# Kernel optimization log

Hardware: AMD Instinct MI355X
Metric: run time of the kernel (lower is better)

Reference implementation:

```python
import jax, jax.numpy as jnp
import numpy as np

BN_EPS = 1e-5      # torch BatchNorm2d default eps
NORM_EPS = 1e-12   # torch F.normalize default eps


def conv1x1_bn(x, W, b, gamma, beta, mean, var):
    # 1x1 conv == channel matmul; BN in eval mode (running stats)
    y = jnp.einsum('oc,nchw->nohw', W, x) + b[None, :, None, None]
    scale = gamma / jnp.sqrt(var + BN_EPS)
    shift = beta - mean * scale
    return y * scale[None, :, None, None] + shift[None, :, None, None]


def _l2norm(x, axis):
    n = jnp.sqrt(jnp.sum(x * x, axis=axis, keepdims=True))
    return x / jnp.maximum(n, NORM_EPS)


def setup_inputs() -> dict:
    key = jax.random.key(0)
    ks = jax.random.split(key, 16)
    N, C, H, W = 16, 64, 256, 256
    QK = 32
    d = {}
    d['x'] = jax.random.normal(ks[0], (N, C, H, W), jnp.float32)
    # Q projection (C -> 32) + BN
    d['Wq'] = jax.random.normal(ks[1], (QK, C), jnp.float32) * (1.0 / np.sqrt(C))
    d['bq'] = jax.random.normal(ks[2], (QK,), jnp.float32) * 0.01
    d['q_gamma'] = jnp.ones((QK,), jnp.float32)
    d['q_beta'] = jnp.zeros((QK,), jnp.float32)
    d['q_mean'] = jax.random.normal(ks[3], (QK,), jnp.float32) * 0.1
    d['q_var'] = jax.random.uniform(ks[4], (QK,), jnp.float32, 0.5, 1.5)
    # K projection (C -> 32) + BN
    d['Wk'] = jax.random.normal(ks[5], (QK, C), jnp.float32) * (1.0 / np.sqrt(C))
    d['bk'] = jax.random.normal(ks[6], (QK,), jnp.float32) * 0.01
    d['k_gamma'] = jnp.ones((QK,), jnp.float32)
    d['k_beta'] = jnp.zeros((QK,), jnp.float32)
    d['k_mean'] = jax.random.normal(ks[7], (QK,), jnp.float32) * 0.1
    d['k_var'] = jax.random.uniform(ks[8], (QK,), jnp.float32, 0.5, 1.5)
    # V projection (C -> C) + BN
    d['Wv'] = jax.random.normal(ks[9], (C, C), jnp.float32) * (1.0 / np.sqrt(C))
    d['bv'] = jax.random.normal(ks[10], (C,), jnp.float32) * 0.01
    d['v_gamma'] = jnp.ones((C,), jnp.float32)
    d['v_beta'] = jnp.zeros((C,), jnp.float32)
    d['v_mean'] = jax.random.normal(ks[11], (C,), jnp.float32) * 0.1
    d['v_var'] = jax.random.uniform(ks[12], (C,), jnp.float32, 0.5, 1.5)
    # output conv-BN-ReLU (C -> C)
    d['Wo'] = jax.random.normal(ks[13], (C, C), jnp.float32) * (1.0 / np.sqrt(C))
    d['bo'] = jax.random.normal(ks[14], (C,), jnp.float32) * 0.01
    d['o_gamma'] = jnp.ones((C,), jnp.float32)
    d['o_beta'] = jnp.zeros((C,), jnp.float32)
    d['o_mean'] = jax.random.normal(ks[15], (C,), jnp.float32) * 0.1
    d['o_var'] = jax.random.uniform(jax.random.fold_in(key, 99), (C,), jnp.float32, 0.5, 1.5)
    return d


def reference(x, Wq, bq, q_gamma, q_beta, q_mean, q_var,
              Wk, bk, k_gamma, k_beta, k_mean, k_var,
              Wv, bv, v_gamma, v_beta, v_mean, v_var,
              Wo, bo, o_gamma, o_beta, o_mean, o_var):
    N, C, H, W = x.shape
    HW = H * W
    Qm = conv1x1_bn(x, Wq, bq, q_gamma, q_beta, q_mean, q_var)   # [N,32,H,W]
    Km = conv1x1_bn(x, Wk, bk, k_gamma, k_beta, k_mean, k_var)   # [N,32,H,W]
    V0 = conv1x1_bn(x, Wv, bv, v_gamma, v_beta, v_mean, v_var)   # [N,C,H,W]

    Q = jnp.transpose(Qm.reshape(N, 32, HW), (0, 2, 1))          # [N,HW,32]
    Q = _l2norm(Q, axis=2)
    K = _l2norm(Km.reshape(N, 32, HW), axis=1)                   # [N,32,HW]
    V = jax.nn.relu(jnp.transpose(V0.reshape(N, C, HW), (0, 2, 1)))  # [N,HW,C]

    f = jnp.einsum('nks,nsc->nkc', K, V)                         # [N,32,C]
    y = jnp.einsum('nsk,nkc->nsc', Q, f)                         # [N,HW,C]
    y = jnp.transpose(y, (0, 2, 1)).reshape(N, C, H, W)

    out = jax.nn.relu(conv1x1_bn(y, Wo, bo, o_gamma, o_beta, o_mean, o_var))
    return out + V0
```

## Files before the change

kernel.cpp:

```cpp
#include <hip/hip_runtime.h>

#define HW 65536
#define NBATCH 16
#define CCH 64
#define QKC 32

#define OFF_WQT 0
#define OFF_BQ  2048
#define OFF_WKT 2080
#define OFF_BK  4128
#define OFF_WVT 4160
#define OFF_BV  8256
#define OFF_WO  8320
#define OFF_BO  12416
#define OFF_F   12544
#define OFF_MT  45312

#define BPN_A 128
#define BPN_B 128
#define NIT_A ((HW / 64) / BPN_A)
#define NIT_B ((HW / 64) / BPN_B)

typedef __attribute__((ext_vector_type(4))) float f32x4;
typedef __attribute__((ext_vector_type(8))) short bf16x8;
typedef __attribute__((ext_vector_type(4))) short bf16x4;

#define MFMA_P(a, b, c) __builtin_amdgcn_mfma_f32_16x16x32_bf16(a, b, c, 0, 0, 0)
#define MFMA_O(a, b, c) __builtin_amdgcn_mfma_f32_16x16x16bf16_1k(a, b, c, 0, 0, 0)

__device__ __forceinline__ short f2bf(float f) {
    __bf16 h = (__bf16)f;
    return __builtin_bit_cast(short, h);
}

__global__ __launch_bounds__(256) void k0_fold(
    const float* __restrict__ Wq, const float* __restrict__ bq,
    const float* __restrict__ qg, const float* __restrict__ qb,
    const float* __restrict__ qm, const float* __restrict__ qv,
    const float* __restrict__ Wk, const float* __restrict__ bk,
    const float* __restrict__ kg, const float* __restrict__ kb,
    const float* __restrict__ km, const float* __restrict__ kvar,
    const float* __restrict__ Wv, const float* __restrict__ bv,
    const float* __restrict__ vg, const float* __restrict__ vb,
    const float* __restrict__ vm, const float* __restrict__ vvar,
    const float* __restrict__ Wo, const float* __restrict__ bo,
    const float* __restrict__ og, const float* __restrict__ ob,
    const float* __restrict__ om, const float* __restrict__ ovar,
    float* __restrict__ ws)
{
    const int idx = blockIdx.x * 256 + threadIdx.x;
    if (idx < 2048) {
        const int c = idx >> 5, i = idx & 31;
        const float s = qg[i] * rsqrtf(qv[i] + 1e-5f);
        ws[OFF_WQT + idx] = Wq[i * 64 + c] * s;
    } else if (idx < 2080) {
        const int i = idx - 2048;
        const float s = qg[i] * rsqrtf(qv[i] + 1e-5f);
        ws[OFF_BQ + i] = bq[i] * s + qb[i] - qm[i] * s;
    } else if (idx < 4128) {
        const int t = idx - 2080;
        const int c = t >> 5, i = t & 31;
        const float s = kg[i] * rsqrtf(kvar[i] + 1e-5f);
        ws[OFF_WKT + t] = Wk[i * 64 + c] * s;
    } else if (idx < 4160) {
        const int i = idx - 4128;
        const float s = kg[i] * rsqrtf(kvar[i] + 1e-5f);
        ws[OFF_BK + i] = bk[i] * s + kb[i] - km[i] * s;
    } else if (idx < 8256) {
        const int t = idx - 4160;
        const int c = t >> 6, o = t & 63;
        const float s = vg[o] * rsqrtf(vvar[o] + 1e-5f);
        ws[OFF_WVT + t] = Wv[o * 64 + c] * s;
    } else if (idx < 8320) {
        const int o = idx - 8256;
        const float s = vg[o] * rsqrtf(vvar[o] + 1e-5f);
        ws[OFF_BV + o] = bv[o] * s + vb[o] - vm[o] * s;
    } else if (idx < 12416) {
        const int t = idx - 8320;
        const int c = t >> 6, j = t & 63;
        const float s = og[c] * rsqrtf(ovar[c] + 1e-5f);
        ws[OFF_WO + t] = Wo[c * 64 + j] * s;
    } else if (idx < 12480) {
        const int c = idx - 12416;
        const float s = og[c] * rsqrtf(ovar[c] + 1e-5f);
        ws[OFF_BO + c] = bo[c] * s + ob[c] - om[c] * s;
    } else if (idx < 12480 + 32768) {
        ws[OFF_F + (idx - 12480)] = 0.0f;
    }
}

__global__ __launch_bounds__(256) void k1_passA(const float* __restrict__ x,
                                                const float* __restrict__ wsc,
                                                float* __restrict__ f)
{
    __shared__ float red[4 * 2048];

    const int tid = threadIdx.x;
    const int w = tid >> 6;
    const int lane = tid & 63;
    const int ln = lane & 15;
    const int lg = lane >> 4;

    const int n = blockIdx.x / BPN_A;
    const int bslot = blockIdx.x % BPN_A;
    const float* xn = x + (size_t)n * CCH * HW;

    bf16x8 wkf[2][2];
#pragma unroll
    for (int kk = 0; kk < 2; kk++)
#pragma unroll
        for (int t = 0; t < 2; t++) {
            bf16x8 a;
#pragma unroll
            for (int j = 0; j < 8; j++)
                a[j] = f2bf(wsc[OFF_WKT + (kk * 32 + lg * 8 + j) * 32 + t * 16 + ln]);
            wkf[kk][t] = a;
        }
    bf16x8 wvf[2][4];
#pragma unroll
    for (int kk = 0; kk < 2; kk++)
#pragma unroll
        for (int t = 0; t < 4; t++) {
            bf16x8 a;
#pragma unroll
            for (int j = 0; j < 8; j++)
                a[j] = f2bf(wsc[OFF_WVT + (kk * 32 + lg * 8 + j) * 64 + t * 16 + ln]);
            wvf[kk][t] = a;
        }
    float bkb[2], bvb[4];
#pragma unroll
    for (int t = 0; t < 2; t++) bkb[t] = wsc[OFF_BK + t * 16 + ln];
#pragma unroll
    for (int t = 0; t < 4; t++) bvb[t] = wsc[OFF_BV + t * 16 + ln];

    f32x4 facc[2][4];
#pragma unroll
    for (int t = 0; t < 2; t++)
#pragma unroll
        for (int vt = 0; vt < 4; vt++) facc[t][vt] = (f32x4){0.f, 0.f, 0.f, 0.f};

    const int span0 = bslot * NIT_A;

    float xf[16];
    {
        const int sbase = span0 * 64 + w * 16;
#pragma unroll
        for (int kk = 0; kk < 2; kk++) {
            const float* xp = xn + (size_t)(kk * 32 + lg * 8) * HW + sbase + ln;
#pragma unroll
            for (int j = 0; j < 8; j++) xf[kk * 8 + j] = xp[j * HW];
        }
    }

#pragma unroll
    for (int it = 0; it < NIT_A; ++it) {
        float xf2[16];
        if (it + 1 < NIT_A) {
            const int sb2 = (span0 + it + 1) * 64 + w * 16;
#pragma unroll
            for (int kk = 0; kk < 2; kk++) {
                const float* xp = xn + (size_t)(kk * 32 + lg * 8) * HW + sb2 + ln;
#pragma unroll
                for (int j = 0; j < 8; j++) xf2[kk * 8 + j] = xp[j * HW];
            }
        }

        bf16x8 xa[2];
#pragma unroll
        for (int kk = 0; kk < 2; kk++)
#pragma unroll
            for (int j = 0; j < 8; j++) xa[kk][j] = f2bf(xf[kk * 8 + j]);

        f32x4 dk[2], dv[4];
#pragma unroll
        for (int t = 0; t < 2; t++) dk[t] = (f32x4){bkb[t], bkb[t], bkb[t], bkb[t]};
#pragma unroll
        for (int t = 0; t < 4; t++) dv[t] = (f32x4){bvb[t], bvb[t], bvb[t], bvb[t]};
#pragma unroll
        for (int kk = 0; kk < 2; kk++) {
#pragma unroll
            for (int t = 0; t < 2; t++) dk[t] = MFMA_P(xa[kk], wkf[kk][t], dk[t]);
#pragma unroll
            for (int t = 0; t < 4; t++) dv[t] = MFMA_P(xa[kk], wvf[kk][t], dv[t]);
        }

        float inv[4];
#pragma unroll
        for (int r = 0; r < 4; r++) {
            float s = dk[0][r] * dk[0][r] + dk[1][r] * dk[1][r];
            s += __shfl_xor(s, 1, 64);
            s += __shfl_xor(s, 2, 64);
            s += __shfl_xor(s, 4, 64);
            s += __shfl_xor(s, 8, 64);
            inv[r] = 1.0f / fmaxf(sqrtf(s), 1e-12f);
        }

        bf16x4 ka[2], vb[4];
#pragma unroll
        for (int t = 0; t < 2; t++)
#pragma unroll
            for (int r = 0; r < 4; r++) ka[t][r] = f2bf(dk[t][r] * inv[r]);
#pragma unroll
        for (int t = 0; t < 4; t++)
#pragma unroll
            for (int r = 0; r < 4; r++) vb[t][r] = f2bf(fmaxf(dv[t][r], 0.0f));

#pragma unroll
        for (int t = 0; t < 2; t++)
#pragma unroll
            for (int vt = 0; vt < 4; vt++)
                facc[t][vt] = MFMA_O(ka[t], vb[vt], facc[t][vt]);

        if (it + 1 < NIT_A) {
#pragma unroll
            for (int i = 0; i < 16; i++) xf[i] = xf2[i];
        }
    }

#pragma unroll
    for (int t = 0; t < 2; t++)
#pragma unroll
        for (int vt = 0; vt < 4; vt++)
#pragma unroll
            for (int r = 0; r < 4; r++)
                red[w * 2048 + (t * 16 + lg * 4 + r) * 64 + vt * 16 + ln] = facc[t][vt][r];
    __syncthreads();
    float* fn = f + n * (QKC * CCH);
    for (int idx = tid; idx < 2048; idx += 256)
        atomicAdd(&fn[idx], red[idx] + red[2048 + idx] + red[4096 + idx] + red[6144 + idx]);
}

__global__ __launch_bounds__(256) void k2_M(const float* __restrict__ wsc,
                                            float* __restrict__ ws)
{
    const int idx = blockIdx.x * 256 + threadIdx.x;
    if (idx >= NBATCH * QKC * CCH) return;
    const int n = idx / (QKC * CCH);
    const int r = idx % (QKC * CCH);
    const int i = r >> 6, c = r & 63;
    const float* wo = wsc + OFF_WO + c * 64;
    const float* fr = wsc + OFF_F + n * 2048 + i * 64;
    float acc = 0.0f;
#pragma unroll
    for (int j = 0; j < 64; j++) acc += wo[j] * fr[j];
    ws[OFF_MT + idx] = acc;
}

__global__ __launch_bounds__(256) void k3_passB(const float* __restrict__ x,
                                               const float* __restrict__ wsc,
                                               float* __restrict__ out)
{
    __shared__ float qt[4][16 * 36];

    const int tid = threadIdx.x;
    const int w = tid >> 6;
    const int lane = tid & 63;
    const int ln = lane & 15;
    const int lg = lane >> 4;

    const int n = NBATCH - 1 - (blockIdx.x / BPN_B);
    const int slot = BPN_B - 1 - (blockIdx.x % BPN_B);
    const float* xn = x + (size_t)n * CCH * HW;
    float* on = out + (size_t)n * CCH * HW;

    bf16x8 wqf[2][2];
#pragma unroll
    for (int kk = 0; kk < 2; kk++)
#pragma unroll
        for (int t = 0; t < 2; t++) {
            bf16x8 a;
#pragma unroll
            for (int j = 0; j < 8; j++)
                a[j] = f2bf(wsc[OFF_WQT + (kk * 32 + lg * 8 + j) * 32 + t * 16 + ln]);
            wqf[kk][t] = a;
        }
    bf16x8 wvf[2][4];
#pragma unroll
    for (int kk = 0; kk < 2; kk++)
#pragma unroll
        for (int t = 0; t < 4; t++) {
            bf16x8 a;
#pragma unroll
            for (int j = 0; j < 8; j++)
                a[j] = f2bf(wsc[OFF_WVT + (kk * 32 + lg * 8 + j) * 64 + t * 16 + ln]);
            wvf[kk][t] = a;
        }
    bf16x8 mtf[4];
#pragma unroll
    for (int t = 0; t < 4; t++) {
        bf16x8 a;
#pragma unroll
        for (int j = 0; j < 8; j++)
            a[j] = f2bf(wsc[OFF_MT + n * 2048 + (lg * 8 + j) * 64 + t * 16 + ln]);
        mtf[t] = a;
    }
    float bqb[2], bvb[4], bob[4];
#pragma unroll
    for (int t = 0; t < 2; t++) bqb[t] = wsc[OFF_BQ + t * 16 + ln];
#pragma unroll
    for (int t = 0; t < 4; t++) bvb[t] = wsc[OFF_BV + t * 16 + ln];
#pragma unroll
    for (int t = 0; t < 4; t++) bob[t] = wsc[OFF_BO + t * 16 + ln];

    const int span0 = slot * NIT_B;

    float xf[16];
    {
        const int sbase = (span0 + NIT_B - 1) * 64 + w * 16;
#pragma unroll
        for (int kk = 0; kk < 2; kk++) {
            const float* xp = xn + (size_t)(kk * 32 + lg * 8) * HW + sbase + ln;
#pragma unroll
            for (int j = 0; j < 8; j++) xf[kk * 8 + j] = xp[j * HW];
        }
    }

#pragma unroll
    for (int it = 0; it < NIT_B; ++it) {
        const int sbase = (span0 + NIT_B - 1 - it) * 64 + w * 16;

        float xf2[16];
        if (it + 1 < NIT_B) {
            const int sb2 = (span0 + NIT_B - 2 - it) * 64 + w * 16;
#pragma unroll
            for (int kk = 0; kk < 2; kk++) {
                const float* xp = xn + (size_t)(kk * 32 + lg * 8) * HW + sb2 + ln;
#pragma unroll
                for (int j = 0; j < 8; j++) xf2[kk * 8 + j] = xp[j * HW];
            }
        }

        bf16x8 xa[2];
#pragma unroll
        for (int kk = 0; kk < 2; kk++)
#pragma unroll
            for (int j = 0; j < 8; j++) xa[kk][j] = f2bf(xf[kk * 8 + j]);

        f32x4 dq[2], dv0[4];
#pragma unroll
        for (int t = 0; t < 2; t++) dq[t] = (f32x4){bqb[t], bqb[t], bqb[t], bqb[t]};
#pragma unroll
        for (int t = 0; t < 4; t++) dv0[t] = (f32x4){bvb[t], bvb[t], bvb[t], bvb[t]};
#pragma unroll
        for (int kk = 0; kk < 2; kk++) {
#pragma unroll
            for (int t = 0; t < 2; t++) dq[t] = MFMA_P(xa[kk], wqf[kk][t], dq[t]);
#pragma unroll
            for (int t = 0; t < 4; t++) dv0[t] = MFMA_P(xa[kk], wvf[kk][t], dv0[t]);
        }

        float inv[4];
#pragma unroll
        for (int r = 0; r < 4; r++) {
            float s = dq[0][r] * dq[0][r] + dq[1][r] * dq[1][r];
            s += __shfl_xor(s, 1, 64);
            s += __shfl_xor(s, 2, 64);
            s += __shfl_xor(s, 4, 64);
            s += __shfl_xor(s, 8, 64);
            inv[r] = 1.0f / fmaxf(sqrtf(s), 1e-12f);
        }

#pragma unroll
        for (int t = 0; t < 2; t++)
#pragma unroll
            for (int r = 0; r < 4; r++)
                qt[w][(lg * 4 + r) * 36 + t * 16 + ln] = dq[t][r] * inv[r];
        const f32x4 qlo = *(const f32x4*)&qt[w][ln * 36 + lg * 8];
        const f32x4 qhi = *(const f32x4*)&qt[w][ln * 36 + lg * 8 + 4];
        bf16x8 aq;
#pragma unroll
        for (int j = 0; j < 4; j++) { aq[j] = f2bf(qlo[j]); aq[4 + j] = f2bf(qhi[j]); }

        f32x4 dy[4];
#pragma unroll
        for (int t = 0; t < 4; t++) dy[t] = (f32x4){bob[t], bob[t], bob[t], bob[t]};
#pragma unroll
        for (int t = 0; t < 4; t++) dy[t] = MFMA_P(aq, mtf[t], dy[t]);

#pragma unroll
        for (int t = 0; t < 4; t++) {
            float* op = on + (size_t)(t * 16 + ln) * HW + sbase + lg * 4;
            f32x4 o4;
#pragma unroll
            for (int r = 0; r < 4; r++)
                o4[r] = fmaxf(dy[t][r], 0.0f) + dv0[t][r];
            __builtin_nontemporal_store(o4, (f32x4*)op);
        }

        if (it + 1 < NIT_B) {
#pragma unroll
            for (int i = 0; i < 16; i++) xf[i] = xf2[i];
        }
    }
}

extern "C" void kernel_launch(void* const* d_in, const int* in_sizes, int n_in,
                              void* d_out, int out_size, void* d_ws, size_t ws_size,
                              hipStream_t stream)
{
    const float* x    = (const float*)d_in[0];
    const float* Wq   = (const float*)d_in[1];
    const float* bq   = (const float*)d_in[2];
    const float* qg   = (const float*)d_in[3];
    const float* qb   = (const float*)d_in[4];
    const float* qm   = (const float*)d_in[5];
    const float* qv   = (const float*)d_in[6];
    const float* Wk   = (const float*)d_in[7];
    const float* bk   = (const float*)d_in[8];
    const float* kg   = (const float*)d_in[9];
    const float* kb   = (const float*)d_in[10];
    const float* km   = (const float*)d_in[11];
    const float* kvar = (const float*)d_in[12];
    const float* Wv   = (const float*)d_in[13];
    const float* bv   = (const float*)d_in[14];
    const float* vg   = (const float*)d_in[15];
    const float* vb   = (const float*)d_in[16];
    const float* vm   = (const float*)d_in[17];
    const float* vvar = (const float*)d_in[18];
    const float* Wo   = (const float*)d_in[19];
    const float* bo   = (const float*)d_in[20];
    const float* og   = (const float*)d_in[21];
    const float* ob   = (const float*)d_in[22];
    const float* om   = (const float*)d_in[23];
    const float* ovar = (const float*)d_in[24];

    float* ws  = (float*)d_ws;
    float* out = (float*)d_out;

    k0_fold<<<177, 256, 0, stream>>>(Wq, bq, qg, qb, qm, qv,
                                     Wk, bk, kg, kb, km, kvar,
                                     Wv, bv, vg, vb, vm, vvar,
                                     Wo, bo, og, ob, om, ovar, ws);

    k1_passA<<<NBATCH * BPN_A, 256, 0, stream>>>(x, (const float*)ws, ws + OFF_F);

    k2_M<<<128, 256, 0, stream>>>((const float*)ws, ws);

    k3_passB<<<NBATCH * BPN_B, 256, 0, stream>>>(x, (const float*)ws, out);
}
```

Before: 185.1 us.

## Stage x tiles through padded LDS with 16-byte coalesced global loads

```diff
diff --git a/kernel.cpp b/kernel.cpp
--- a/kernel.cpp
+++ b/kernel.cpp
@@ -18,8 +18,10 @@
 
 #define BPN_A 128
 #define BPN_B 128
-#define NIT_A ((HW / 64) / BPN_A)
-#define NIT_B ((HW / 64) / BPN_B)
+#define CHUNK_PX 128
+#define SP 129
+#define NIT_A (HW / CHUNK_PX / BPN_A)
+#define NIT_B (HW / CHUNK_PX / BPN_B)
 
 typedef __attribute__((ext_vector_type(4))) float f32x4;
 typedef __attribute__((ext_vector_type(8))) short bf16x8;
@@ -27,6 +29,12 @@
 
 #define MFMA_P(a, b, c) __builtin_amdgcn_mfma_f32_16x16x32_bf16(a, b, c, 0, 0, 0)
 #define MFMA_O(a, b, c) __builtin_amdgcn_mfma_f32_16x16x16bf16_1k(a, b, c, 0, 0, 0)
+
+#define LDS_BARRIER()                                          \
+    do {                                                       \
+        asm volatile("s_waitcnt lgkmcnt(0)" ::: "memory");     \
+        __builtin_amdgcn_s_barrier();                          \
+    } while (0)
 
 __device__ __forceinline__ short f2bf(float f) {
     __bf16 h = (__bf16)f;
@@ -93,13 +101,15 @@
                                                 const float* __restrict__ wsc,
                                                 float* __restrict__ f)
 {
-    __shared__ float red[4 * 2048];
+    __shared__ float lds[64 * SP];
 
     const int tid = threadIdx.x;
     const int w = tid >> 6;
     const int lane = tid & 63;
     const int ln = lane & 15;
     const int lg = lane >> 4;
+    const int lc = tid >> 5;
+    const int lpx = (tid & 31) * 4;
 
     const int n = blockIdx.x / BPN_A;
     const int bslot = blockIdx.x % BPN_A;
@@ -141,82 +151,84 @@
 
     const int span0 = bslot * NIT_A;
 
-    float xf[16];
-    {
-        const int sbase = span0 * 64 + w * 16;
-#pragma unroll
-        for (int kk = 0; kk < 2; kk++) {
-            const float* xp = xn + (size_t)(kk * 32 + lg * 8) * HW + sbase + ln;
-#pragma unroll
-            for (int j = 0; j < 8; j++) xf[kk * 8 + j] = xp[j * HW];
+    f32x4 L[8];
+#pragma unroll
+    for (int r = 0; r < 8; ++r)
+        L[r] = *(const f32x4*)(xn + (size_t)(r * 8 + lc) * HW + span0 * CHUNK_PX + lpx);
+
+#pragma unroll 1
+    for (int it = 0; it < NIT_A; ++it) {
+#pragma unroll
+        for (int r = 0; r < 8; ++r) {
+            const int c = r * 8 + lc;
+#pragma unroll
+            for (int e = 0; e < 4; ++e)
+                lds[c * SP + lpx + e] = L[r][e];
+        }
+        if (it + 1 < NIT_A) {
+            const int bp = (span0 + it + 1) * CHUNK_PX;
+#pragma unroll
+            for (int r = 0; r < 8; ++r)
+                L[r] = *(const f32x4*)(xn + (size_t)(r * 8 + lc) * HW + bp + lpx);
+        }
+        LDS_BARRIER();
+
+        bf16x8 xag[2][2];
+#pragma unroll
+        for (int kk = 0; kk < 2; kk++)
+#pragma unroll
+            for (int j = 0; j < 8; j++) {
+                const int c = kk * 32 + lg * 8 + j;
+                xag[0][kk][j] = f2bf(lds[c * SP + (w * 32) + ln]);
+                xag[1][kk][j] = f2bf(lds[c * SP + (w * 32 + 16) + ln]);
+            }
+        LDS_BARRIER();
+
+#pragma unroll
+        for (int g = 0; g < 2; ++g) {
+            f32x4 dk[2], dv[4];
+#pragma unroll
+            for (int t = 0; t < 2; t++) dk[t] = (f32x4){bkb[t], bkb[t], bkb[t], bkb[t]};
+#pragma unroll
+            for (int t = 0; t < 4; t++) dv[t] = (f32x4){bvb[t], bvb[t], bvb[t], bvb[t]};
+#pragma unroll
+            for (int kk = 0; kk < 2; kk++) {
+#pragma unroll
+                for (int t = 0; t < 2; t++) dk[t] = MFMA_P(xag[g][kk], wkf[kk][t], dk[t]);
+#pragma unroll
+                for (int t = 0; t < 4; t++) dv[t] = MFMA_P(xag[g][kk], wvf[kk][t], dv[t]);
+            }
+
+            float inv[4];
+#pragma unroll
+            for (int r = 0; r < 4; r++) {
+                float s = dk[0][r] * dk[0][r] + dk[1][r] * dk[1][r];
+                s += __shfl_xor(s, 1, 64);
+                s += __shfl_xor(s, 2, 64);
+                s += __shfl_xor(s, 4, 64);
+                s += __shfl_xor(s, 8, 64);
+                inv[r] = 1.0f / fmaxf(sqrtf(s), 1e-12f);
+            }
+
+            bf16x4 ka[2], vb[4];
+#pragma unroll
+            for (int t = 0; t < 2; t++)
+#pragma unroll
+                for (int r = 0; r < 4; r++) ka[t][r] = f2bf(dk[t][r] * inv[r]);
+#pragma unroll
+            for (int t = 0; t < 4; t++)
+#pragma unroll
+                for (int r = 0; r < 4; r++) vb[t][r] = f2bf(fmaxf(dv[t][r], 0.0f));
+
+#pragma unroll
+            for (int t = 0; t < 2; t++)
+#pragma unroll
+                for (int vt = 0; vt < 4; vt++)
+                    facc[t][vt] = MFMA_O(ka[t], vb[vt], facc[t][vt]);
         }
     }
 
-#pragma unroll
-    for (int it = 0; it < NIT_A; ++it) {
-        float xf2[16];
-        if (it + 1 < NIT_A) {
-            const int sb2 = (span0 + it + 1) * 64 + w * 16;
-#pragma unroll
-            for (int kk = 0; kk < 2; kk++) {
-                const float* xp = xn + (size_t)(kk * 32 + lg * 8) * HW + sb2 + ln;
-#pragma unroll
-                for (int j = 0; j < 8; j++) xf2[kk * 8 + j] = xp[j * HW];
-            }
-        }
-
-        bf16x8 xa[2];
-#pragma unroll
-        for (int kk = 0; kk < 2; kk++)
-#pragma unroll
-            for (int j = 0; j < 8; j++) xa[kk][j] = f2bf(xf[kk * 8 + j]);
-
-        f32x4 dk[2], dv[4];
-#pragma unroll
-        for (int t = 0; t < 2; t++) dk[t] = (f32x4){bkb[t], bkb[t], bkb[t], bkb[t]};
-#pragma unroll
-        for (int t = 0; t < 4; t++) dv[t] = (f32x4){bvb[t], bvb[t], bvb[t], bvb[t]};
-#pragma unroll
-        for (int kk = 0; kk < 2; kk++) {
-#pragma unroll
-            for (int t = 0; t < 2; t++) dk[t] = MFMA_P(xa[kk], wkf[kk][t], dk[t]);
-#pragma unroll
-            for (int t = 0; t < 4; t++) dv[t] = MFMA_P(xa[kk], wvf[kk][t], dv[t]);
-        }
-
-        float inv[4];
-#pragma unroll
-        for (int r = 0; r < 4; r++) {
-            float s = dk[0][r] * dk[0][r] + dk[1][r] * dk[1][r];
-            s += __shfl_xor(s, 1, 64);
-            s += __shfl_xor(s, 2, 64);
-            s += __shfl_xor(s, 4, 64);
-            s += __shfl_xor(s, 8, 64);
-            inv[r] = 1.0f / fmaxf(sqrtf(s), 1e-12f);
-        }
-
-        bf16x4 ka[2], vb[4];
-#pragma unroll
-        for (int t = 0; t < 2; t++)
-#pragma unroll
-            for (int r = 0; r < 4; r++) ka[t][r] = f2bf(dk[t][r] * inv[r]);
-#pragma unroll
-        for (int t = 0; t < 4; t++)
-#pragma unroll
-            for (int r = 0; r < 4; r++) vb[t][r] = f2bf(fmaxf(dv[t][r], 0.0f));
-
-#pragma unroll
-        for (int t = 0; t < 2; t++)
-#pragma unroll
-            for (int vt = 0; vt < 4; vt++)
-                facc[t][vt] = MFMA_O(ka[t], vb[vt], facc[t][vt]);
-
-        if (it + 1 < NIT_A) {
-#pragma unroll
-            for (int i = 0; i < 16; i++) xf[i] = xf2[i];
-        }
-    }
-
+    float* red = lds;
 #pragma unroll
     for (int t = 0; t < 2; t++)
 #pragma unroll
@@ -250,6 +262,7 @@
                                                const float* __restrict__ wsc,
                                                float* __restrict__ out)
 {
+    __shared__ float xt[64 * SP];
     __shared__ float qt[4][16 * 36];
 
     const int tid = threadIdx.x;
@@ -257,6 +270,8 @@
     const int lane = tid & 63;
     const int ln = lane & 15;
     const int lg = lane >> 4;
+    const int lc = tid >> 5;
+    const int lpx = (tid & 31) * 4;
 
     const int n = NBATCH - 1 - (blockIdx.x / BPN_B);
     const int slot = BPN_B - 1 - (blockIdx.x % BPN_B);
@@ -304,92 +319,98 @@
 
     const int span0 = slot * NIT_B;
 
-    float xf[16];
+    f32x4 L[8];
     {
-        const int sbase = (span0 + NIT_B - 1) * 64 + w * 16;
-#pragma unroll
-        for (int kk = 0; kk < 2; kk++) {
-            const float* xp = xn + (size_t)(kk * 32 + lg * 8) * HW + sbase + ln;
-#pragma unroll
-            for (int j = 0; j < 8; j++) xf[kk * 8 + j] = xp[j * HW];
-        }
+        const int bp = (span0 + NIT_B - 1) * CHUNK_PX;
+#pragma unroll
+        for (int r = 0; r < 8; ++r)
+            L[r] = *(const f32x4*)(xn + (size_t)(r * 8 + lc) * HW + bp + lpx);
     }
 
-#pragma unroll
+#pragma unroll 1
     for (int it = 0; it < NIT_B; ++it) {
-        const int sbase = (span0 + NIT_B - 1 - it) * 64 + w * 16;
-
-        float xf2[16];
+        const int base_px = (span0 + NIT_B - 1 - it) * CHUNK_PX;
+
+#pragma unroll
+        for (int r = 0; r < 8; ++r) {
+            const int c = r * 8 + lc;
+#pragma unroll
+            for (int e = 0; e < 4; ++e)
+                xt[c * SP + lpx + e] = L[r][e];
+        }
         if (it + 1 < NIT_B) {
-            const int sb2 = (span0 + NIT_B - 2 - it) * 64 + w * 16;
+            const int bp = (span0 + NIT_B - 2 - it) * CHUNK_PX;
+#pragma unroll
+            for (int r = 0; r < 8; ++r)
+                L[r] = *(const f32x4*)(xn + (size_t)(r * 8 + lc) * HW + bp + lpx);
+        }
+        LDS_BARRIER();
+
+        bf16x8 xag[2][2];
+#pragma unroll
+        for (int kk = 0; kk < 2; kk++)
+#pragma unroll
+            for (int j = 0; j < 8; j++) {
+                const int c = kk * 32 + lg * 8 + j;
+                xag[0][kk][j] = f2bf(xt[c * SP + (w * 32) + ln]);
+                xag[1][kk][j] = f2bf(xt[c * SP + (w * 32 + 16) + ln]);
+            }
+        LDS_BARRIER();
+
+#pragma unroll
+        for (int g = 0; g < 2; ++g) {
+            const int abs_px = base_px + w * 32 + g * 16;
+
+            f32x4 dq[2], dv0[4];
+#pragma unroll
+            for (int t = 0; t < 2; t++) dq[t] = (f32x4){bqb[t], bqb[t], bqb[t], bqb[t]};
+#pragma unroll
+            for (int t = 0; t < 4; t++) dv0[t] = (f32x4){bvb[t], bvb[t], bvb[t], bvb[t]};
 #pragma unroll
             for (int kk = 0; kk < 2; kk++) {
-                const float* xp = xn + (size_t)(kk * 32 + lg * 8) * HW + sb2 + ln;
-#pragma unroll
-                for (int j = 0; j < 8; j++) xf2[kk * 8 + j] = xp[j * HW];
-            }
-        }
-
-        bf16x8 xa[2];
-#pragma unroll
-        for (int kk = 0; kk < 2; kk++)
-#pragma unroll
-            for (int j = 0; j < 8; j++) xa[kk][j] = f2bf(xf[kk * 8 + j]);
-
-        f32x4 dq[2], dv0[4];
-#pragma unroll
-        for (int t = 0; t < 2; t++) dq[t] = (f32x4){bqb[t], bqb[t], bqb[t], bqb[t]};
-#pragma unroll
-        for (int t = 0; t < 4; t++) dv0[t] = (f32x4){bvb[t], bvb[t], bvb[t], bvb[t]};
-#pragma unroll
-        for (int kk = 0; kk < 2; kk++) {
-#pragma unroll
-            for (int t = 0; t < 2; t++) dq[t] = MFMA_P(xa[kk], wqf[kk][t], dq[t]);
-#pragma unroll
-            for (int t = 0; t < 4; t++) dv0[t] = MFMA_P(xa[kk], wvf[kk][t], dv0[t]);
-        }
-
-        float inv[4];
-#pragma unroll
-        for (int r = 0; r < 4; r++) {
-            float s = dq[0][r] * dq[0][r] + dq[1][r] * dq[1][r];
-            s += __shfl_xor(s, 1, 64);
-            s += __shfl_xor(s, 2, 64);
-            s += __shfl_xor(s, 4, 64);
-            s += __shfl_xor(s, 8, 64);
-            inv[r] = 1.0f / fmaxf(sqrtf(s), 1e-12f);
-        }
-
-#pragma unroll
-        for (int t = 0; t < 2; t++)
-#pragma unroll
-            for (int r = 0; r < 4; r++)
-                qt[w][(lg * 4 + r) * 36 + t * 16 + ln] = dq[t][r] * inv[r];
-        const f32x4 qlo = *(const f32x4*)&qt[w][ln * 36 + lg * 8];
-        const f32x4 qhi = *(const f32x4*)&qt[w][ln * 36 + lg * 8 + 4];
-        bf16x8 aq;
-#pragma unroll
-        for (int j = 0; j < 4; j++) { aq[j] = f2bf(qlo[j]); aq[4 + j] = f2bf(qhi[j]); }
-
-        f32x4 dy[4];
-#pragma unroll
-        for (int t = 0; t < 4; t++) dy[t] = (f32x4){bob[t], bob[t], bob[t], bob[t]};
-#pragma unroll
-        for (int t = 0; t < 4; t++) dy[t] = MFMA_P(aq, mtf[t], dy[t]);
-
-#pragma unroll
-        for (int t = 0; t < 4; t++) {
-            float* op = on + (size_t)(t * 16 + ln) * HW + sbase + lg * 4;
-            f32x4 o4;
-#pragma unroll
-            for (int r = 0; r < 4; r++)
-                o4[r] = fmaxf(dy[t][r], 0.0f) + dv0[t][r];
-            __builtin_nontemporal_store(o4, (f32x4*)op);
-        }
-
-        if (it + 1 < NIT_B) {
-#pragma unroll
-            for (int i = 0; i < 16; i++) xf[i] = xf2[i];
+#pragma unroll
+                for (int t = 0; t < 2; t++) dq[t] = MFMA_P(xag[g][kk], wqf[kk][t], dq[t]);
+#pragma unroll
+                for (int t = 0; t < 4; t++) dv0[t] = MFMA_P(xag[g][kk], wvf[kk][t], dv0[t]);
+            }
+
+            float inv[4];
+#pragma unroll
+            for (int r = 0; r < 4; r++) {
+                float s = dq[0][r] * dq[0][r] + dq[1][r] * dq[1][r];
+                s += __shfl_xor(s, 1, 64);
+                s += __shfl_xor(s, 2, 64);
+                s += __shfl_xor(s, 4, 64);
+                s += __shfl_xor(s, 8, 64);
+                inv[r] = 1.0f / fmaxf(sqrtf(s), 1e-12f);
+            }
+
+#pragma unroll
+            for (int t = 0; t < 2; t++)
+#pragma unroll
+                for (int r = 0; r < 4; r++)
+                    qt[w][(lg * 4 + r) * 36 + t * 16 + ln] = dq[t][r] * inv[r];
+            const f32x4 qlo = *(const f32x4*)&qt[w][ln * 36 + lg * 8];
+            const f32x4 qhi = *(const f32x4*)&qt[w][ln * 36 + lg * 8 + 4];
+            bf16x8 aq;
+#pragma unroll
+            for (int j = 0; j < 4; j++) { aq[j] = f2bf(qlo[j]); aq[4 + j] = f2bf(qhi[j]); }
+
+            f32x4 dy[4];
+#pragma unroll
+            for (int t = 0; t < 4; t++) dy[t] = (f32x4){bob[t], bob[t], bob[t], bob[t]};
+#pragma unroll
+            for (int t = 0; t < 4; t++) dy[t] = MFMA_P(aq, mtf[t], dy[t]);
+
+#pragma unroll
+            for (int t = 0; t < 4; t++) {
+                float* op = on + (size_t)(t * 16 + ln) * HW + abs_px + lg * 4;
+                f32x4 o4;
+#pragma unroll
+                for (int r = 0; r < 4; r++)
+                    o4[r] = fmaxf(dy[t][r], 0.0f) + dv0[t][r];
+                __builtin_nontemporal_store(o4, (f32x4*)op);
+            }
         }
     }
 }
```

Result: slower. 223.5 us (+20.8%).

## Vectorize kernel A x loads to float2, process two pixel groups per iteration, cut blocks per batch

Applied to the files above, without the earlier changes.

```diff
diff --git a/kernel.cpp b/kernel.cpp
--- a/kernel.cpp
+++ b/kernel.cpp
@@ -16,11 +16,12 @@
 #define OFF_F   12544
 #define OFF_MT  45312
 
-#define BPN_A 128
-#define BPN_B 128
-#define NIT_A ((HW / 64) / BPN_A)
-#define NIT_B ((HW / 64) / BPN_B)
-
+#define BPN_A 32
+#define BPN_B 32
+#define NIT_A (HW / 128 / BPN_A)
+#define NIT_B (HW / 64 / BPN_B)
+
+typedef __attribute__((ext_vector_type(2))) float f32x2;
 typedef __attribute__((ext_vector_type(4))) float f32x4;
 typedef __attribute__((ext_vector_type(8))) short bf16x8;
 typedef __attribute__((ext_vector_type(4))) short bf16x4;
@@ -141,75 +142,81 @@
 
     const int span0 = bslot * NIT_A;
 
-    float xf[16];
+    f32x2 xf[16];
     {
-        const int sbase = span0 * 64 + w * 16;
-#pragma unroll
-        for (int kk = 0; kk < 2; kk++) {
-            const float* xp = xn + (size_t)(kk * 32 + lg * 8) * HW + sbase + ln;
-#pragma unroll
-            for (int j = 0; j < 8; j++) xf[kk * 8 + j] = xp[j * HW];
-        }
-    }
-
-#pragma unroll
+        const int base = span0 * 128 + w * 32;
+#pragma unroll
+        for (int kk = 0; kk < 2; kk++)
+#pragma unroll
+            for (int j = 0; j < 8; j++)
+                xf[kk * 8 + j] = *(const f32x2*)(xn + (size_t)(kk * 32 + lg * 8 + j) * HW
+                                                 + base + 2 * ln);
+    }
+
+#pragma unroll 1
     for (int it = 0; it < NIT_A; ++it) {
-        float xf2[16];
+        f32x2 xf2[16];
         if (it + 1 < NIT_A) {
-            const int sb2 = (span0 + it + 1) * 64 + w * 16;
+            const int b2 = (span0 + it + 1) * 128 + w * 32;
+#pragma unroll
+            for (int kk = 0; kk < 2; kk++)
+#pragma unroll
+                for (int j = 0; j < 8; j++)
+                    xf2[kk * 8 + j] = *(const f32x2*)(xn + (size_t)(kk * 32 + lg * 8 + j) * HW
+                                                      + b2 + 2 * ln);
+        }
+
+        bf16x8 xag[2][2];
+#pragma unroll
+        for (int e = 0; e < 2; e++)
+#pragma unroll
+            for (int kk = 0; kk < 2; kk++)
+#pragma unroll
+                for (int j = 0; j < 8; j++)
+                    xag[e][kk][j] = f2bf(xf[kk * 8 + j][e]);
+
+#pragma unroll
+        for (int g = 0; g < 2; ++g) {
+            f32x4 dk[2], dv[4];
+#pragma unroll
+            for (int t = 0; t < 2; t++) dk[t] = (f32x4){bkb[t], bkb[t], bkb[t], bkb[t]};
+#pragma unroll
+            for (int t = 0; t < 4; t++) dv[t] = (f32x4){bvb[t], bvb[t], bvb[t], bvb[t]};
 #pragma unroll
             for (int kk = 0; kk < 2; kk++) {
-                const float* xp = xn + (size_t)(kk * 32 + lg * 8) * HW + sb2 + ln;
-#pragma unroll
-                for (int j = 0; j < 8; j++) xf2[kk * 8 + j] = xp[j * HW];
+#pragma unroll
+                for (int t = 0; t < 2; t++) dk[t] = MFMA_P(xag[g][kk], wkf[kk][t], dk[t]);
+#pragma unroll
+                for (int t = 0; t < 4; t++) dv[t] = MFMA_P(xag[g][kk], wvf[kk][t], dv[t]);
             }
-        }
-
-        bf16x8 xa[2];
-#pragma unroll
-        for (int kk = 0; kk < 2; kk++)
-#pragma unroll
-            for (int j = 0; j < 8; j++) xa[kk][j] = f2bf(xf[kk * 8 + j]);
-
-        f32x4 dk[2], dv[4];
-#pragma unroll
-        for (int t = 0; t < 2; t++) dk[t] = (f32x4){bkb[t], bkb[t], bkb[t], bkb[t]};
-#pragma unroll
-        for (int t = 0; t < 4; t++) dv[t] = (f32x4){bvb[t], bvb[t], bvb[t], bvb[t]};
-#pragma unroll
-        for (int kk = 0; kk < 2; kk++) {
-#pragma unroll
-            for (int t = 0; t < 2; t++) dk[t] = MFMA_P(xa[kk], wkf[kk][t], dk[t]);
-#pragma unroll
-            for (int t = 0; t < 4; t++) dv[t] = MFMA_P(xa[kk], wvf[kk][t], dv[t]);
-        }
-
-        float inv[4];
-#pragma unroll
-        for (int r = 0; r < 4; r++) {
-            float s = dk[0][r] * dk[0][r] + dk[1][r] * dk[1][r];
-            s += __shfl_xor(s, 1, 64);
-            s += __shfl_xor(s, 2, 64);
-            s += __shfl_xor(s, 4, 64);
-            s += __shfl_xor(s, 8, 64);
-            inv[r] = 1.0f / fmaxf(sqrtf(s), 1e-12f);
-        }
-
-        bf16x4 ka[2], vb[4];
-#pragma unroll
-        for (int t = 0; t < 2; t++)
-#pragma unroll
-            for (int r = 0; r < 4; r++) ka[t][r] = f2bf(dk[t][r] * inv[r]);
-#pragma unroll
-        for (int t = 0; t < 4; t++)
-#pragma unroll
-            for (int r = 0; r < 4; r++) vb[t][r] = f2bf(fmaxf(dv[t][r], 0.0f));
-
-#pragma unroll
-        for (int t = 0; t < 2; t++)
-#pragma unroll
-            for (int vt = 0; vt < 4; vt++)
-                facc[t][vt] = MFMA_O(ka[t], vb[vt], facc[t][vt]);
+
+            float inv[4];
+#pragma unroll
+            for (int r = 0; r < 4; r++) {
+                float s = dk[0][r] * dk[0][r] + dk[1][r] * dk[1][r];
+                s += __shfl_xor(s, 1, 64);
+                s += __shfl_xor(s, 2, 64);
+                s += __shfl_xor(s, 4, 64);
+                s += __shfl_xor(s, 8, 64);
+                inv[r] = 1.0f / fmaxf(sqrtf(s), 1e-12f);
+            }
+
+            bf16x4 ka[2], vb[4];
+#pragma unroll
+            for (int t = 0; t < 2; t++)
+#pragma unroll
+                for (int r = 0; r < 4; r++) ka[t][r] = f2bf(dk[t][r] * inv[r]);
+#pragma unroll
+            for (int t = 0; t < 4; t++)
+#pragma unroll
+                for (int r = 0; r < 4; r++) vb[t][r] = f2bf(fmaxf(dv[t][r], 0.0f));
+
+#pragma unroll
+            for (int t = 0; t < 2; t++)
+#pragma unroll
+                for (int vt = 0; vt < 4; vt++)
+                    facc[t][vt] = MFMA_O(ka[t], vb[vt], facc[t][vt]);
+        }
 
         if (it + 1 < NIT_A) {
 #pragma unroll
@@ -315,7 +322,7 @@
         }
     }
 
-#pragma unroll
+#pragma unroll 1
     for (int it = 0; it < NIT_B; ++it) {
         const int sbase = (span0 + NIT_B - 1 - it) * 64 + w * 16;
 
```

Result: no change. 186.4 us (+0.7%).
